# Kernel optimization log

Measured on AMD Instinct MI355X. Metric: run time of the kernel, lower is better.

## Reference

```python
import jax, jax.numpy as jnp
import numpy as np

N, CH = 65536, 256
B, K, CTX = 8, 256, 768
H, D = 8, 64
NPB = N // B  # points per batch (scene)


def setup_inputs() -> dict:
    key = jax.random.key(0)
    ks = jax.random.split(key, 8)
    xF = jax.random.normal(ks[0], (N, CH), dtype=jnp.float32)
    context = jax.random.normal(ks[1], (B, K, CTX), dtype=jnp.float32)
    # decomposition_permutations: a random partition of the N sparse points into B groups
    perm = jax.random.permutation(ks[2], N).reshape(B, NPB).astype(jnp.int32)
    Wq = jax.random.normal(ks[3], (CH, H * D), dtype=jnp.float32) * 0.02
    Wk = jax.random.normal(ks[4], (CTX, H * D), dtype=jnp.float32) * 0.02
    Wv = jax.random.normal(ks[5], (CTX, H * D), dtype=jnp.float32) * 0.02
    Wout = jax.random.normal(ks[6], (H * D, CH), dtype=jnp.float32) * 0.02
    b_out = jnp.zeros((CH,), dtype=jnp.float32)
    return {"xF": xF, "context": context, "perm": perm,
            "Wq": Wq, "Wk": Wk, "Wv": Wv, "Wout": Wout, "b_out": b_out}


def reference(xF, context, perm, Wq, Wk, Wv, Wout, b_out):
    scale = D ** -0.5
    q = (xF @ Wq).reshape(N, H, D)                     # to_q (1x1 conv == linear)
    k = (context @ Wk).reshape(B, K, H, D)             # to_k
    v = (context @ Wv).reshape(B, K, H, D)             # to_v
    qg = q[perm]                                        # gather: [B, NPB, H, D]
    attn = jax.nn.softmax(scale * jnp.einsum('bqhd,bkhd->bhqk', qg, k), axis=-1)
    o = jnp.einsum('bhqk,bkhd->bqhd', attn, v).reshape(B * NPB, H * D)
    # inverse-permutation scatter back to sparse-tensor order: ft[inv_perm]
    ft = jnp.zeros((N, H * D), o.dtype).at[perm.reshape(-1)].set(o)
    out = ft @ Wout + b_out                             # to_out
    return out + xF                                     # residual
```

## Files before the change

### kernel.cpp

```cpp
#include <hip/hip_runtime.h>

typedef unsigned short u16;
typedef __attribute__((ext_vector_type(8))) short bf16x8;
typedef __attribute__((ext_vector_type(4))) float f32x4;
typedef __attribute__((ext_vector_type(4))) int i32x4;
typedef __attribute__((ext_vector_type(2))) int i32x2;

#define N_PTS   65536
#define CH_DIM  256
#define BATCH   8
#define KTOK    256
#define CTX_DIM 768
#define NHEAD   8
#define HD      64
#define HDIM    512
#define NPB     8192

__device__ __forceinline__ u16 f2bf(float f) {
    union { float f; unsigned u; } v; v.f = f;
    unsigned r = v.u + 0x7fffu + ((v.u >> 16) & 1u);
    return (u16)(r >> 16);
}
__device__ __forceinline__ unsigned cvtpk(float lo, float hi) {
    unsigned r;
    asm("v_cvt_pk_bf16_f32 %0, %1, %2" : "=v"(r) : "v"(lo), "v"(hi));
    return r;
}
__device__ __forceinline__ float exp2_hw(float x) {
    float r;
    asm("v_exp_f32 %0, %1" : "=v"(r) : "v"(x));
    return r;
}
__device__ __forceinline__ float max3f(float a, float b, float c) {
    float r;
    asm("v_max3_f32 %0, %1, %2, %3" : "=v"(r) : "v"(a), "v"(b), "v"(c));
    return r;
}

__device__ __forceinline__ void gll16(const void* g, void* l) {
    __builtin_amdgcn_global_load_lds(
        (const __attribute__((address_space(1))) void*)g,
        (__attribute__((address_space(3))) void*)l, 16, 0, 0);
}

__global__ void convk(const float* __restrict__ src, u16* __restrict__ dst, int n8) {
    int i = blockIdx.x * blockDim.x + threadIdx.x;
    int st = gridDim.x * blockDim.x;
    for (; i < n8; i += st) {
        const float* p = src + (size_t)i * 8;
        f32x4 a = *(const f32x4*)p;
        f32x4 b = *(const f32x4*)(p + 4);
        i32x4 o;
        o[0] = (int)cvtpk(a[0], a[1]);
        o[1] = (int)cvtpk(a[2], a[3]);
        o[2] = (int)cvtpk(b[0], b[1]);
        o[3] = (int)cvtpk(b[2], b[3]);
        *(i32x4*)&dst[(size_t)i * 8] = o;
    }
}

__global__ void tconvk(const float* __restrict__ W, u16* __restrict__ WT, int R, int C) {
    int i = blockIdx.x * blockDim.x + threadIdx.x;
    if (i >= R * C) return;
    WT[i] = f2bf(W[(size_t)(i % R) * C + i / R]);
}

__global__ void tconv3k(const float* __restrict__ Wq, const float* __restrict__ Wk,
                        const float* __restrict__ Wv,
                        u16* __restrict__ WqT, u16* __restrict__ WkvT) {
    int i = blockIdx.x * blockDim.x + threadIdx.x;
    if (i < 131072) {
        WqT[i] = f2bf(Wq[(size_t)(i % 256) * 512 + i / 256]);
    } else if (i < 524288) {
        int j = i - 131072;
        WkvT[j] = f2bf(Wk[(size_t)(j % 768) * 512 + j / 768]);
    } else if (i < 917504) {
        int j = i - 524288;
        WkvT[393216 + j] = f2bf(Wv[(size_t)(j % 768) * 512 + j / 768]);
    }
}

template <int KC, bool OUT_F32>
__global__ __launch_bounds__(256, 3) void gemm_bt(
    const u16* __restrict__ A, const u16* __restrict__ BT, void* __restrict__ Cv,
    int M, int N,
    const float* __restrict__ bias, const float* __restrict__ resid, float oscale)
{
    __shared__ __align__(16) u16 As[2][128 * 32];
    __shared__ __align__(16) u16 Bs[2][128 * 32];

    const int tid  = threadIdx.x;
    const int lane = tid & 63;
    const int w    = tid >> 6;
    const int wm   = w & 1;
    const int wn   = w >> 1;

    const int nwg = gridDim.x * gridDim.y;
    const int wg  = blockIdx.y * gridDim.x + blockIdx.x;
    const int swz = (wg & 7) * (nwg >> 3) + (wg >> 3);
    const int n0  = (swz % gridDim.x) * 128;
    const int m0  = (swz / gridDim.x) * 128;

    const int l15  = lane & 15;
    const int quad = lane >> 4;

    f32x4 acc[4][4];
#pragma unroll
    for (int i = 0; i < 4; i++)
#pragma unroll
        for (int j = 0; j < 4; j++) { acc[i][j][0]=0.f; acc[i][j][1]=0.f; acc[i][j][2]=0.f; acc[i][j][3]=0.f; }

    const int sr = tid >> 2;
    const int sc = (tid & 3) * 8;
    const u16* Abase = A  + (size_t)(m0 + sr) * KC + sc;
    const u16* Bbase = BT + (size_t)(n0 + sr) * KC + sc;
    const size_t rowStep = (size_t)64 * KC;
    const int d8 = tid * 8;

    gll16(Abase,           &As[0][d8]);
    gll16(Abase + rowStep, &As[0][d8 + 2048]);
    gll16(Bbase,           &Bs[0][d8]);
    gll16(Bbase + rowStep, &Bs[0][d8 + 2048]);
    asm volatile("s_waitcnt vmcnt(0)" ::: "memory");
    __builtin_amdgcn_s_barrier();
    __builtin_amdgcn_sched_barrier(0);

    constexpr int ntile = KC >> 5;
    int cur = 0;
    for (int t = 0; t < ntile; ++t) {
        if (t + 1 < ntile) {
            const u16* An = Abase + ((t + 1) << 5);
            const u16* Bn = Bbase + ((t + 1) << 5);
            const int nxt = cur ^ 1;
            gll16(An,           &As[nxt][d8]);
            gll16(An + rowStep, &As[nxt][d8 + 2048]);
            gll16(Bn,           &Bs[nxt][d8]);
            gll16(Bn + rowStep, &Bs[nxt][d8 + 2048]);
        }
        bf16x8 af[4], bfr[4];
#pragma unroll
        for (int rt = 0; rt < 4; rt++)
            af[rt] = *(const bf16x8*)&As[cur][(wm * 64 + rt * 16 + l15) * 32 + quad * 8];
#pragma unroll
        for (int nt = 0; nt < 4; nt++)
            bfr[nt] = *(const bf16x8*)&Bs[cur][(wn * 64 + nt * 16 + l15) * 32 + quad * 8];
#pragma unroll
        for (int rt = 0; rt < 4; rt++)
#pragma unroll
            for (int nt = 0; nt < 4; nt++)
                acc[rt][nt] = __builtin_amdgcn_mfma_f32_16x16x32_bf16(bfr[nt], af[rt], acc[rt][nt], 0, 0, 0);
        asm volatile("s_waitcnt vmcnt(0)" ::: "memory");
        __builtin_amdgcn_sched_barrier(0);
        __builtin_amdgcn_s_barrier();
        __builtin_amdgcn_sched_barrier(0);
        cur ^= 1;
    }

    if (OUT_F32) {
#pragma unroll
        for (int rt = 0; rt < 4; rt++) {
            int m = m0 + wm * 64 + rt * 16 + l15;
#pragma unroll
            for (int nt = 0; nt < 4; nt++) {
                int nb = n0 + wn * 64 + nt * 16 + quad * 4;
                f32x4 v  = acc[rt][nt];
                f32x4 bv = *(const f32x4*)&bias[nb];
                f32x4 rv = *(const f32x4*)&resid[(size_t)m * N + nb];
#pragma unroll
                for (int r = 0; r < 4; r++) v[r] += bv[r] + rv[r];
                *(f32x4*)&((float*)Cv)[(size_t)m * N + nb] = v;
            }
        }
    } else {
#pragma unroll
        for (int rt = 0; rt < 4; rt++) {
            int m = m0 + wm * 64 + rt * 16 + l15;
#pragma unroll
            for (int nt = 0; nt < 4; nt++) {
                int nb = n0 + wn * 64 + nt * 16 + quad * 4;
                union { unsigned u[2]; i32x2 q; } pk;
                pk.u[0] = cvtpk(acc[rt][nt][0] * oscale, acc[rt][nt][1] * oscale);
                pk.u[1] = cvtpk(acc[rt][nt][2] * oscale, acc[rt][nt][3] * oscale);
                *(i32x2*)&((u16*)Cv)[(size_t)m * N + nb] = pk.q;
            }
        }
    }
}

__global__ __launch_bounds__(256, 4) void gemm_kv(
    const u16* __restrict__ A, const u16* __restrict__ BT,
    u16* __restrict__ kd, u16* __restrict__ vtd)
{
    __shared__ __align__(16) u16 As[2][64 * 32];
    __shared__ __align__(16) u16 Bs[2][64 * 32];
    const int K = CTX_DIM;

    const int tid  = threadIdx.x;
    const int lane = tid & 63;
    const int w    = tid >> 6;
    const int wm   = w & 1;
    const int wn   = w >> 1;

    const int nwg = gridDim.x * gridDim.y;
    const int wg  = blockIdx.y * gridDim.x + blockIdx.x;
    const int swz = (wg & 7) * (nwg >> 3) + (wg >> 3);
    const int n0  = (swz % gridDim.x) * 64;
    const int m0  = (swz / gridDim.x) * 64;

    const int l15  = lane & 15;
    const int quad = lane >> 4;

    f32x4 acc[2][2];
#pragma unroll
    for (int i = 0; i < 2; i++)
#pragma unroll
        for (int j = 0; j < 2; j++) { acc[i][j][0]=0.f; acc[i][j][1]=0.f; acc[i][j][2]=0.f; acc[i][j][3]=0.f; }

    const int sr = tid >> 2;
    const int sc = (tid & 3) * 8;
    const u16* Abase = A  + (size_t)(m0 + sr) * K + sc;
    const u16* Bbase = BT + (size_t)(n0 + sr) * K + sc;
    const int d8 = tid * 8;

    gll16(Abase, &As[0][d8]);
    gll16(Bbase, &Bs[0][d8]);
    asm volatile("s_waitcnt vmcnt(0)" ::: "memory");
    __builtin_amdgcn_s_barrier();
    __builtin_amdgcn_sched_barrier(0);

    const int ntile = K >> 5;
    int cur = 0;
    for (int t = 0; t < ntile; ++t) {
        if (t + 1 < ntile) {
            const int nxt = cur ^ 1;
            gll16(Abase + ((t + 1) << 5), &As[nxt][d8]);
            gll16(Bbase + ((t + 1) << 5), &Bs[nxt][d8]);
        }
        bf16x8 af[2], bfr[2];
#pragma unroll
        for (int rt = 0; rt < 2; rt++)
            af[rt] = *(const bf16x8*)&As[cur][(wm * 32 + rt * 16 + l15) * 32 + quad * 8];
#pragma unroll
        for (int nt = 0; nt < 2; nt++)
            bfr[nt] = *(const bf16x8*)&Bs[cur][(wn * 32 + nt * 16 + l15) * 32 + quad * 8];
#pragma unroll
        for (int rt = 0; rt < 2; rt++)
#pragma unroll
            for (int nt = 0; nt < 2; nt++)
                acc[rt][nt] = __builtin_amdgcn_mfma_f32_16x16x32_bf16(af[rt], bfr[nt], acc[rt][nt], 0, 0, 0);
        asm volatile("s_waitcnt vmcnt(0)" ::: "memory");
        __builtin_amdgcn_sched_barrier(0);
        __builtin_amdgcn_s_barrier();
        __builtin_amdgcn_sched_barrier(0);
        cur ^= 1;
    }

    if (n0 < 512) {
#pragma unroll
        for (int nt = 0; nt < 2; nt++) {
            int col = n0 + wn * 32 + nt * 16 + l15;
#pragma unroll
            for (int rt = 0; rt < 2; rt++) {
#pragma unroll
                for (int r = 0; r < 4; r++) {
                    int row = m0 + wm * 32 + rt * 16 + quad * 4 + r;
                    kd[(size_t)row * HDIM + col] = f2bf(acc[rt][nt][r]);
                }
            }
        }
    } else {
#pragma unroll
        for (int nt = 0; nt < 2; nt++) {
            int col = (n0 - 512) + wn * 32 + nt * 16 + l15;
            int hh = col >> 6, dd = col & 63;
#pragma unroll
            for (int rt = 0; rt < 2; rt++) {
                int row = m0 + wm * 32 + rt * 16 + quad * 4;
                int bb = row >> 8, jb = row & 255;
                int jp = (jb & 0xE0) | ((jb & 0x0C) << 1) | ((jb & 0x10) >> 2);
                union { unsigned u[2]; i32x2 q; } pk;
                pk.u[0] = cvtpk(acc[rt][nt][0], acc[rt][nt][1]);
                pk.u[1] = cvtpk(acc[rt][nt][2], acc[rt][nt][3]);
                *(i32x2*)&vtd[(((size_t)(bb * 8 + hh)) * 64 + dd) * 256 + jp] = pk.q;
            }
        }
    }
}

#define KS2 72
#define VS2 264
__global__ __launch_bounds__(256, 4) void attn_mfma(
    const u16* qbuf, const u16* __restrict__ kbuf,
    const u16* __restrict__ vbufT, const int* __restrict__ perm,
    u16* ft)
{
    __shared__ __align__(16) u16 smem[18432];
    u16* Ks = smem;
    u16* Vt = smem;

    const int tid   = threadIdx.x;
    const int lane  = tid & 63;
    const int w     = tid >> 6;
    const int chunk = blockIdx.x;
    const int bh    = blockIdx.y;
    const int b     = bh >> 3;
    const int h     = bh & 7;
    const int l15   = lane & 15;
    const int quad  = lane >> 4;

    const int prow = perm[b * NPB + chunk * 64 + w * 16 + l15];
    const u16* qrow = qbuf + (size_t)prow * HDIM + h * HD;
    bf16x8 qf0 = *(const bf16x8*)&qrow[quad * 8];
    bf16x8 qf1 = *(const bf16x8*)&qrow[32 + quad * 8];

    {
        const int j8 = tid >> 3;
        const int c  = (tid & 7) * 8;
#pragma unroll
        for (int pass = 0; pass < 8; pass++) {
            int jj = j8 + pass * 32;
            i32x4 val = *(const i32x4*)&kbuf[((size_t)(b * KTOK + jj)) * HDIM + h * HD + c];
            *(i32x4*)&Ks[jj * KS2 + c] = val;
        }
    }
    __syncthreads();

    f32x4 sc[16];
#pragma unroll
    for (int nt = 0; nt < 16; nt++) { sc[nt][0]=0.f; sc[nt][1]=0.f; sc[nt][2]=0.f; sc[nt][3]=0.f; }
#pragma unroll
    for (int nt = 0; nt < 16; nt++) {
        bf16x8 kf = *(const bf16x8*)&Ks[(nt * 16 + l15) * KS2 + quad * 8];
        sc[nt] = __builtin_amdgcn_mfma_f32_16x16x32_bf16(kf, qf0, sc[nt], 0, 0, 0);
    }
#pragma unroll
    for (int nt = 0; nt < 16; nt++) {
        bf16x8 kf = *(const bf16x8*)&Ks[(nt * 16 + l15) * KS2 + 32 + quad * 8];
        sc[nt] = __builtin_amdgcn_mfma_f32_16x16x32_bf16(kf, qf1, sc[nt], 0, 0, 0);
    }

    i32x4 vreg[8];
    const u16* vslice = vbufT + ((size_t)(b * NHEAD + h)) * HD * KTOK;
    const int vrow = tid >> 2;
    const int vc0  = (tid & 3) * 8;
#pragma unroll
    for (int pass = 0; pass < 8; pass++)
        vreg[pass] = *(const i32x4*)&vslice[(size_t)vrow * KTOK + vc0 + pass * 32];

    float m = -1e30f;
#pragma unroll
    for (int nt = 0; nt < 16; nt++) {
        f32x4 v = sc[nt];
        m = max3f(m, max3f(v[0], v[1], v[2]), v[3]);
    }
    m = fmaxf(m, __shfl_xor(m, 16));
    m = fmaxf(m, __shfl_xor(m, 32));
    float s0 = 0.f, s1 = 0.f, s2 = 0.f, s3 = 0.f;
#pragma unroll
    for (int nt = 0; nt < 16; nt++) {
        float e0 = exp2_hw(sc[nt][0] - m);
        float e1 = exp2_hw(sc[nt][1] - m);
        float e2 = exp2_hw(sc[nt][2] - m);
        float e3 = exp2_hw(sc[nt][3] - m);
        sc[nt][0] = e0; sc[nt][1] = e1; sc[nt][2] = e2; sc[nt][3] = e3;
        s0 += e0; s1 += e1; s2 += e2; s3 += e3;
    }
    float s = (s0 + s1) + (s2 + s3);
    s += __shfl_xor(s, 16);
    s += __shfl_xor(s, 32);
    float inv = 1.0f / s;

    unsigned up[16][2];
#pragma unroll
    for (int nt = 0; nt < 16; nt++) {
        up[nt][0] = cvtpk(sc[nt][0], sc[nt][1]);
        up[nt][1] = cvtpk(sc[nt][2], sc[nt][3]);
    }

    __syncthreads();

#pragma unroll
    for (int pass = 0; pass < 8; pass++)
        *(i32x4*)&Vt[vrow * VS2 + vc0 + pass * 32] = vreg[pass];
    __syncthreads();

    f32x4 o[4];
#pragma unroll
    for (int n = 0; n < 4; n++) { o[n][0]=0.f; o[n][1]=0.f; o[n][2]=0.f; o[n][3]=0.f; }

#pragma unroll
    for (int ks = 0; ks < 8; ks++) {
        union { unsigned u[4]; bf16x8 v; } pb;
        pb.u[0] = up[2 * ks][0];
        pb.u[1] = up[2 * ks][1];
        pb.u[2] = up[2 * ks + 1][0];
        pb.u[3] = up[2 * ks + 1][1];
#pragma unroll
        for (int nt = 0; nt < 4; nt++) {
            bf16x8 av = *(const bf16x8*)&Vt[(nt * 16 + l15) * VS2 + ks * 32 + quad * 8];
            o[nt] = __builtin_amdgcn_mfma_f32_16x16x32_bf16(av, pb.v, o[nt], 0, 0, 0);
        }
    }

    {
        u16* frow = ft + (size_t)prow * HDIM + h * HD;
#pragma unroll
        for (int nt = 0; nt < 4; nt++) {
            union { unsigned u[2]; i32x2 q; } pk;
            pk.u[0] = cvtpk(o[nt][0] * inv, o[nt][1] * inv);
            pk.u[1] = cvtpk(o[nt][2] * inv, o[nt][3] * inv);
            *(i32x2*)&frow[nt * 16 + quad * 4] = pk.q;
        }
    }
}

extern "C" void kernel_launch(void* const* d_in, const int* in_sizes, int n_in,
                              void* d_out, int out_size, void* d_ws, size_t ws_size,
                              hipStream_t stream) {
    const float* xF      = (const float*)d_in[0];
    const float* context = (const float*)d_in[1];
    const int*   perm    = (const int*)d_in[2];
    const float* Wq      = (const float*)d_in[3];
    const float* Wk      = (const float*)d_in[4];
    const float* Wv      = (const float*)d_in[5];
    const float* Wout    = (const float*)d_in[6];
    const float* b_out   = (const float*)d_in[7];
    float*       out     = (float*)d_out;

    const size_t WS_NEED = 71303168ULL;
    if (ws_size < WS_NEED) {
        hipMemsetAsync(d_out, 0, (size_t)out_size * sizeof(float), stream);
        return;
    }
    char* ws    = (char*)d_ws;
    u16* kbuf   = (u16*)(ws + 0);
    u16* vbufT  = (u16*)(ws + 2097152);
    u16* qbuf   = (u16*)(ws + 4194304);
    u16* ft     = qbuf;
    u16* WoutT  = (u16*)(ws + 2097152);

    char* ob    = (char*)d_out;
    u16* xb     = (u16*)(ob + 0);
    u16* cb     = (u16*)(ob + 33554432);
    u16* WkvT   = (u16*)(ob + 36700160);
    u16* WqT    = (u16*)(ob + 38273024);

    convk<<<2048, 256, 0, stream>>>(xF, xb, N_PTS * CH_DIM / 8);
    convk<<<768, 256, 0, stream>>>(context, cb, BATCH * KTOK * CTX_DIM / 8);
    tconv3k<<<3584, 256, 0, stream>>>(Wq, Wk, Wv, WqT, WkvT);

    gemm_bt<CH_DIM, false><<<dim3(HDIM / 128, N_PTS / 128), 256, 0, stream>>>(
        xb, WqT, qbuf, N_PTS, HDIM, nullptr, nullptr, 0.1803368801f);
    gemm_kv<<<dim3(16, 32), 256, 0, stream>>>(cb, WkvT, kbuf, vbufT);

    attn_mfma<<<dim3(NPB / 64, BATCH * NHEAD), 256, 0, stream>>>(
        qbuf, kbuf, vbufT, perm, ft);

    tconvk<<<(HDIM * CH_DIM + 255) / 256, 256, 0, stream>>>(Wout, WoutT, HDIM, CH_DIM);
    gemm_bt<HDIM, true><<<dim3(CH_DIM / 128, N_PTS / 128), 256, 0, stream>>>(
        ft, WoutT, out, N_PTS, CH_DIM, b_out, xF, 1.0f);
}
```

Baseline: 292.1 us.

## Fuse output projection, bias and residual into the attention kernel

New measurement: 365.8 us. 25.2% more time.

```diff
diff --git a/kernel.cpp b/kernel.cpp
--- a/kernel.cpp
+++ b/kernel.cpp
@@ -59,15 +59,10 @@
     }
 }
 
-__global__ void tconvk(const float* __restrict__ W, u16* __restrict__ WT, int R, int C) {
-    int i = blockIdx.x * blockDim.x + threadIdx.x;
-    if (i >= R * C) return;
-    WT[i] = f2bf(W[(size_t)(i % R) * C + i / R]);
-}
-
-__global__ void tconv3k(const float* __restrict__ Wq, const float* __restrict__ Wk,
-                        const float* __restrict__ Wv,
-                        u16* __restrict__ WqT, u16* __restrict__ WkvT) {
+__global__ void tconv4k(const float* __restrict__ Wq, const float* __restrict__ Wk,
+                        const float* __restrict__ Wv, const float* __restrict__ Wo,
+                        u16* __restrict__ WqT, u16* __restrict__ WkvT,
+                        u16* __restrict__ WoT) {
     int i = blockIdx.x * blockDim.x + threadIdx.x;
     if (i < 131072) {
         WqT[i] = f2bf(Wq[(size_t)(i % 256) * 512 + i / 256]);
@@ -77,14 +72,16 @@
     } else if (i < 917504) {
         int j = i - 524288;
         WkvT[393216 + j] = f2bf(Wv[(size_t)(j % 768) * 512 + j / 768]);
-    }
-}
-
-template <int KC, bool OUT_F32>
+    } else if (i < 1048576) {
+        int j = i - 917504;
+        WoT[j] = f2bf(Wo[(size_t)(j % 512) * 256 + j / 512]);
+    }
+}
+
+template <int KC>
 __global__ __launch_bounds__(256, 3) void gemm_bt(
     const u16* __restrict__ A, const u16* __restrict__ BT, void* __restrict__ Cv,
-    int M, int N,
-    const float* __restrict__ bias, const float* __restrict__ resid, float oscale)
+    int M, int N, float oscale)
 {
     __shared__ __align__(16) u16 As[2][128 * 32];
     __shared__ __align__(16) u16 Bs[2][128 * 32];
@@ -156,33 +153,16 @@
         cur ^= 1;
     }
 
-    if (OUT_F32) {
-#pragma unroll
-        for (int rt = 0; rt < 4; rt++) {
-            int m = m0 + wm * 64 + rt * 16 + l15;
-#pragma unroll
-            for (int nt = 0; nt < 4; nt++) {
-                int nb = n0 + wn * 64 + nt * 16 + quad * 4;
-                f32x4 v  = acc[rt][nt];
-                f32x4 bv = *(const f32x4*)&bias[nb];
-                f32x4 rv = *(const f32x4*)&resid[(size_t)m * N + nb];
-#pragma unroll
-                for (int r = 0; r < 4; r++) v[r] += bv[r] + rv[r];
-                *(f32x4*)&((float*)Cv)[(size_t)m * N + nb] = v;
-            }
-        }
-    } else {
-#pragma unroll
-        for (int rt = 0; rt < 4; rt++) {
-            int m = m0 + wm * 64 + rt * 16 + l15;
-#pragma unroll
-            for (int nt = 0; nt < 4; nt++) {
-                int nb = n0 + wn * 64 + nt * 16 + quad * 4;
-                union { unsigned u[2]; i32x2 q; } pk;
-                pk.u[0] = cvtpk(acc[rt][nt][0] * oscale, acc[rt][nt][1] * oscale);
-                pk.u[1] = cvtpk(acc[rt][nt][2] * oscale, acc[rt][nt][3] * oscale);
-                *(i32x2*)&((u16*)Cv)[(size_t)m * N + nb] = pk.q;
-            }
+#pragma unroll
+    for (int rt = 0; rt < 4; rt++) {
+        int m = m0 + wm * 64 + rt * 16 + l15;
+#pragma unroll
+        for (int nt = 0; nt < 4; nt++) {
+            int nb = n0 + wn * 64 + nt * 16 + quad * 4;
+            union { unsigned u[2]; i32x2 q; } pk;
+            pk.u[0] = cvtpk(acc[rt][nt][0] * oscale, acc[rt][nt][1] * oscale);
+            pk.u[1] = cvtpk(acc[rt][nt][2] * oscale, acc[rt][nt][3] * oscale);
+            *(i32x2*)&((u16*)Cv)[(size_t)m * N + nb] = pk.q;
         }
     }
 }
@@ -289,128 +269,150 @@
 
 #define KS2 72
 #define VS2 264
-__global__ __launch_bounds__(256, 4) void attn_mfma(
+#define OS2 72
+__global__ __launch_bounds__(256, 2) void attn_out(
     const u16* qbuf, const u16* __restrict__ kbuf,
     const u16* __restrict__ vbufT, const int* __restrict__ perm,
-    u16* ft)
+    const u16* __restrict__ WoT, const float* __restrict__ bias,
+    const float* __restrict__ resid, float* out)
 {
-    __shared__ __align__(16) u16 smem[18432];
+    __shared__ __align__(16) u16 smem[23040];
     u16* Ks = smem;
     u16* Vt = smem;
+    u16* Os = smem + 18432;
 
     const int tid   = threadIdx.x;
     const int lane  = tid & 63;
     const int w     = tid >> 6;
     const int chunk = blockIdx.x;
-    const int bh    = blockIdx.y;
-    const int b     = bh >> 3;
-    const int h     = bh & 7;
+    const int b     = blockIdx.y;
     const int l15   = lane & 15;
     const int quad  = lane >> 4;
 
     const int prow = perm[b * NPB + chunk * 64 + w * 16 + l15];
-    const u16* qrow = qbuf + (size_t)prow * HDIM + h * HD;
-    bf16x8 qf0 = *(const bf16x8*)&qrow[quad * 8];
-    bf16x8 qf1 = *(const bf16x8*)&qrow[32 + quad * 8];
-
-    {
-        const int j8 = tid >> 3;
-        const int c  = (tid & 7) * 8;
+    const u16* qrow = qbuf + (size_t)prow * HDIM;
+
+    f32x4 acc_out[16];
+#pragma unroll
+    for (int i = 0; i < 16; i++) { acc_out[i][0]=0.f; acc_out[i][1]=0.f; acc_out[i][2]=0.f; acc_out[i][3]=0.f; }
+
+    const int j8 = tid >> 3;
+    const int c  = (tid & 7) * 8;
+    const int vrow = tid >> 2;
+    const int vc0  = (tid & 3) * 8;
+
+    for (int h = 0; h < NHEAD; ++h) {
 #pragma unroll
         for (int pass = 0; pass < 8; pass++) {
             int jj = j8 + pass * 32;
             i32x4 val = *(const i32x4*)&kbuf[((size_t)(b * KTOK + jj)) * HDIM + h * HD + c];
             *(i32x4*)&Ks[jj * KS2 + c] = val;
         }
-    }
-    __syncthreads();
-
-    f32x4 sc[16];
-#pragma unroll
-    for (int nt = 0; nt < 16; nt++) { sc[nt][0]=0.f; sc[nt][1]=0.f; sc[nt][2]=0.f; sc[nt][3]=0.f; }
-#pragma unroll
-    for (int nt = 0; nt < 16; nt++) {
-        bf16x8 kf = *(const bf16x8*)&Ks[(nt * 16 + l15) * KS2 + quad * 8];
-        sc[nt] = __builtin_amdgcn_mfma_f32_16x16x32_bf16(kf, qf0, sc[nt], 0, 0, 0);
-    }
-#pragma unroll
-    for (int nt = 0; nt < 16; nt++) {
-        bf16x8 kf = *(const bf16x8*)&Ks[(nt * 16 + l15) * KS2 + 32 + quad * 8];
-        sc[nt] = __builtin_amdgcn_mfma_f32_16x16x32_bf16(kf, qf1, sc[nt], 0, 0, 0);
-    }
-
-    i32x4 vreg[8];
-    const u16* vslice = vbufT + ((size_t)(b * NHEAD + h)) * HD * KTOK;
-    const int vrow = tid >> 2;
-    const int vc0  = (tid & 3) * 8;
-#pragma unroll
-    for (int pass = 0; pass < 8; pass++)
-        vreg[pass] = *(const i32x4*)&vslice[(size_t)vrow * KTOK + vc0 + pass * 32];
-
-    float m = -1e30f;
-#pragma unroll
-    for (int nt = 0; nt < 16; nt++) {
-        f32x4 v = sc[nt];
-        m = max3f(m, max3f(v[0], v[1], v[2]), v[3]);
-    }
-    m = fmaxf(m, __shfl_xor(m, 16));
-    m = fmaxf(m, __shfl_xor(m, 32));
-    float s0 = 0.f, s1 = 0.f, s2 = 0.f, s3 = 0.f;
-#pragma unroll
-    for (int nt = 0; nt < 16; nt++) {
-        float e0 = exp2_hw(sc[nt][0] - m);
-        float e1 = exp2_hw(sc[nt][1] - m);
-        float e2 = exp2_hw(sc[nt][2] - m);
-        float e3 = exp2_hw(sc[nt][3] - m);
-        sc[nt][0] = e0; sc[nt][1] = e1; sc[nt][2] = e2; sc[nt][3] = e3;
-        s0 += e0; s1 += e1; s2 += e2; s3 += e3;
-    }
-    float s = (s0 + s1) + (s2 + s3);
-    s += __shfl_xor(s, 16);
-    s += __shfl_xor(s, 32);
-    float inv = 1.0f / s;
-
-    unsigned up[16][2];
-#pragma unroll
-    for (int nt = 0; nt < 16; nt++) {
-        up[nt][0] = cvtpk(sc[nt][0], sc[nt][1]);
-        up[nt][1] = cvtpk(sc[nt][2], sc[nt][3]);
-    }
-
-    __syncthreads();
-
-#pragma unroll
-    for (int pass = 0; pass < 8; pass++)
-        *(i32x4*)&Vt[vrow * VS2 + vc0 + pass * 32] = vreg[pass];
-    __syncthreads();
-
-    f32x4 o[4];
-#pragma unroll
-    for (int n = 0; n < 4; n++) { o[n][0]=0.f; o[n][1]=0.f; o[n][2]=0.f; o[n][3]=0.f; }
-
-#pragma unroll
-    for (int ks = 0; ks < 8; ks++) {
-        union { unsigned u[4]; bf16x8 v; } pb;
-        pb.u[0] = up[2 * ks][0];
-        pb.u[1] = up[2 * ks][1];
-        pb.u[2] = up[2 * ks + 1][0];
-        pb.u[3] = up[2 * ks + 1][1];
-#pragma unroll
-        for (int nt = 0; nt < 4; nt++) {
-            bf16x8 av = *(const bf16x8*)&Vt[(nt * 16 + l15) * VS2 + ks * 32 + quad * 8];
-            o[nt] = __builtin_amdgcn_mfma_f32_16x16x32_bf16(av, pb.v, o[nt], 0, 0, 0);
-        }
-    }
-
-    {
-        u16* frow = ft + (size_t)prow * HDIM + h * HD;
+        __syncthreads();
+
+        bf16x8 qf0 = *(const bf16x8*)&qrow[h * HD + quad * 8];
+        bf16x8 qf1 = *(const bf16x8*)&qrow[h * HD + 32 + quad * 8];
+
+        f32x4 sc[16];
+#pragma unroll
+        for (int nt = 0; nt < 16; nt++) { sc[nt][0]=0.f; sc[nt][1]=0.f; sc[nt][2]=0.f; sc[nt][3]=0.f; }
+#pragma unroll
+        for (int nt = 0; nt < 16; nt++) {
+            bf16x8 kf = *(const bf16x8*)&Ks[(nt * 16 + l15) * KS2 + quad * 8];
+            sc[nt] = __builtin_amdgcn_mfma_f32_16x16x32_bf16(kf, qf0, sc[nt], 0, 0, 0);
+        }
+#pragma unroll
+        for (int nt = 0; nt < 16; nt++) {
+            bf16x8 kf = *(const bf16x8*)&Ks[(nt * 16 + l15) * KS2 + 32 + quad * 8];
+            sc[nt] = __builtin_amdgcn_mfma_f32_16x16x32_bf16(kf, qf1, sc[nt], 0, 0, 0);
+        }
+
+        i32x4 vreg[8];
+        const u16* vslice = vbufT + ((size_t)(b * NHEAD + h)) * HD * KTOK;
+#pragma unroll
+        for (int pass = 0; pass < 8; pass++)
+            vreg[pass] = *(const i32x4*)&vslice[(size_t)vrow * KTOK + vc0 + pass * 32];
+
+        float m = -1e30f;
+#pragma unroll
+        for (int nt = 0; nt < 16; nt++) {
+            f32x4 v = sc[nt];
+            m = max3f(m, max3f(v[0], v[1], v[2]), v[3]);
+        }
+        m = fmaxf(m, __shfl_xor(m, 16));
+        m = fmaxf(m, __shfl_xor(m, 32));
+        float s0 = 0.f, s1 = 0.f, s2 = 0.f, s3 = 0.f;
+        unsigned up[16][2];
+#pragma unroll
+        for (int nt = 0; nt < 16; nt++) {
+            float e0 = exp2_hw(sc[nt][0] - m);
+            float e1 = exp2_hw(sc[nt][1] - m);
+            float e2 = exp2_hw(sc[nt][2] - m);
+            float e3 = exp2_hw(sc[nt][3] - m);
+            up[nt][0] = cvtpk(e0, e1);
+            up[nt][1] = cvtpk(e2, e3);
+            s0 += e0; s1 += e1; s2 += e2; s3 += e3;
+        }
+        float s = (s0 + s1) + (s2 + s3);
+        s += __shfl_xor(s, 16);
+        s += __shfl_xor(s, 32);
+        float inv = 1.0f / s;
+
+        __syncthreads();
+
+#pragma unroll
+        for (int pass = 0; pass < 8; pass++)
+            *(i32x4*)&Vt[vrow * VS2 + vc0 + pass * 32] = vreg[pass];
+        __syncthreads();
+
+        f32x4 o[4];
+#pragma unroll
+        for (int n = 0; n < 4; n++) { o[n][0]=0.f; o[n][1]=0.f; o[n][2]=0.f; o[n][3]=0.f; }
+#pragma unroll
+        for (int ks = 0; ks < 8; ks++) {
+            union { unsigned u[4]; bf16x8 v; } pb;
+            pb.u[0] = up[2 * ks][0];
+            pb.u[1] = up[2 * ks][1];
+            pb.u[2] = up[2 * ks + 1][0];
+            pb.u[3] = up[2 * ks + 1][1];
+#pragma unroll
+            for (int nt = 0; nt < 4; nt++) {
+                bf16x8 av = *(const bf16x8*)&Vt[(nt * 16 + l15) * VS2 + ks * 32 + quad * 8];
+                o[nt] = __builtin_amdgcn_mfma_f32_16x16x32_bf16(av, pb.v, o[nt], 0, 0, 0);
+            }
+        }
+
 #pragma unroll
         for (int nt = 0; nt < 4; nt++) {
             union { unsigned u[2]; i32x2 q; } pk;
             pk.u[0] = cvtpk(o[nt][0] * inv, o[nt][1] * inv);
             pk.u[1] = cvtpk(o[nt][2] * inv, o[nt][3] * inv);
-            *(i32x2*)&frow[nt * 16 + quad * 4] = pk.q;
-        }
+            *(i32x2*)&Os[(w * 16 + l15) * OS2 + nt * 16 + quad * 4] = pk.q;
+        }
+
+#pragma unroll
+        for (int kk = 0; kk < 2; kk++) {
+            bf16x8 of = *(const bf16x8*)&Os[(w * 16 + l15) * OS2 + kk * 32 + quad * 8];
+#pragma unroll
+            for (int ct = 0; ct < 16; ct++) {
+                bf16x8 wf = *(const bf16x8*)&WoT[(size_t)(ct * 16 + l15) * HDIM + h * HD + kk * 32 + quad * 8];
+                acc_out[ct] = __builtin_amdgcn_mfma_f32_16x16x32_bf16(wf, of, acc_out[ct], 0, 0, 0);
+            }
+        }
+        __syncthreads();
+    }
+
+    const float* xrow = resid + (size_t)prow * CH_DIM;
+    float* orow = out + (size_t)prow * CH_DIM;
+#pragma unroll
+    for (int ct = 0; ct < 16; ct++) {
+        int nb = ct * 16 + quad * 4;
+        f32x4 v  = acc_out[ct];
+        f32x4 bv = *(const f32x4*)&bias[nb];
+        f32x4 rv = *(const f32x4*)&xrow[nb];
+#pragma unroll
+        for (int r = 0; r < 4; r++) v[r] += bv[r] + rv[r];
+        *(f32x4*)&orow[nb] = v;
     }
 }
 
@@ -435,28 +437,22 @@
     char* ws    = (char*)d_ws;
     u16* kbuf   = (u16*)(ws + 0);
     u16* vbufT  = (u16*)(ws + 2097152);
-    u16* qbuf   = (u16*)(ws + 4194304);
-    u16* ft     = qbuf;
-    u16* WoutT  = (u16*)(ws + 2097152);
-
-    char* ob    = (char*)d_out;
-    u16* xb     = (u16*)(ob + 0);
-    u16* cb     = (u16*)(ob + 33554432);
-    u16* WkvT   = (u16*)(ob + 36700160);
-    u16* WqT    = (u16*)(ob + 38273024);
+    u16* xb     = (u16*)(ws + 4194304);
+    u16* cb     = (u16*)(ws + 37748736);
+    u16* WkvT   = (u16*)(ws + 40894464);
+    u16* WqT    = (u16*)(ws + 42467328);
+    u16* WoT    = (u16*)(ws + 42729472);
+
+    u16* qbuf   = (u16*)d_out;
 
     convk<<<2048, 256, 0, stream>>>(xF, xb, N_PTS * CH_DIM / 8);
     convk<<<768, 256, 0, stream>>>(context, cb, BATCH * KTOK * CTX_DIM / 8);
-    tconv3k<<<3584, 256, 0, stream>>>(Wq, Wk, Wv, WqT, WkvT);
-
-    gemm_bt<CH_DIM, false><<<dim3(HDIM / 128, N_PTS / 128), 256, 0, stream>>>(
-        xb, WqT, qbuf, N_PTS, HDIM, nullptr, nullptr, 0.1803368801f);
+    tconv4k<<<4096, 256, 0, stream>>>(Wq, Wk, Wv, Wout, WqT, WkvT, WoT);
+
+    gemm_bt<CH_DIM><<<dim3(HDIM / 128, N_PTS / 128), 256, 0, stream>>>(
+        xb, WqT, qbuf, N_PTS, HDIM, 0.1803368801f);
     gemm_kv<<<dim3(16, 32), 256, 0, stream>>>(cb, WkvT, kbuf, vbufT);
 
-    attn_mfma<<<dim3(NPB / 64, BATCH * NHEAD), 256, 0, stream>>>(
-        qbuf, kbuf, vbufT, perm, ft);
-
-    tconvk<<<(HDIM * CH_DIM + 255) / 256, 256, 0, stream>>>(Wout, WoutT, HDIM, CH_DIM);
-    gemm_bt<HDIM, true><<<dim3(CH_DIM / 128, N_PTS / 128), 256, 0, stream>>>(
-        ft, WoutT, out, N_PTS, CH_DIM, b_out, xF, 1.0f);
-}
+    attn_out<<<dim3(NPB / 64, BATCH), 256, 0, stream>>>(
+        qbuf, kbuf, vbufT, perm, WoT, b_out, xF, out);
+}
```
